# Kernel optimization log

Measured on AMD Instinct MI355X. Metric: run time of the kernel, lower is better.

Reference implementation:

```python
import jax, jax.numpy as jnp
import numpy as np
import math

B, T, D_MODEL = 1, 2048, 256
N_Q, N_KV = 16, 1
D_HEAD = D_MODEL // N_KV          # 256 (module forces d_head = d_model // n_kv_heads)
QPG = N_Q // N_KV                 # 16
ROPE_BASE = 10000.0
WINDOW = 512
EPS = 1.1920929e-07               # torch finfo(float32).eps (nn.RMSNorm default eps=None)
NEG = -1e30


def _rope(x, base=ROPE_BASE):
    # x: (b, q, g, t, d); interleaved-pair rotary embedding, freq shared per pair
    t, d = x.shape[-2], x.shape[-1]
    freqs = base ** (-2.0 * jnp.arange(d // 2, dtype=jnp.float32) / d)      # (d/2,)
    theta = jnp.arange(t, dtype=jnp.float32)[:, None] * freqs[None, :]     # (t, d/2)
    cos, sin = jnp.cos(theta), jnp.sin(theta)
    x1, x2 = x[..., 0::2], x[..., 1::2]
    r1 = x1 * cos - x2 * sin
    r2 = x1 * sin + x2 * cos
    return jnp.stack([r1, r2], axis=-1).reshape(x.shape)


def _rmsnorm(x, w):
    return x * jax.lax.rsqrt(jnp.mean(x * x, axis=-1, keepdims=True) + EPS) * w


def setup_inputs() -> dict:
    key = jax.random.key(0)
    k0, k1, k2, k3 = jax.random.split(key, 4)
    x = jax.random.normal(k0, (B, T, D_MODEL), dtype=jnp.float32)
    wq = jax.random.normal(k1, (QPG * N_KV * D_HEAD, D_MODEL), dtype=jnp.float32) * 0.02
    wkv = jax.random.normal(k2, (2 * D_HEAD * N_KV, D_MODEL), dtype=jnp.float32) * 0.02
    wo = jax.random.normal(k3, (D_MODEL, D_HEAD * N_Q * N_KV), dtype=jnp.float32) * 0.02
    q_norm_w = jnp.ones((D_HEAD,), dtype=jnp.float32)
    k_norm_w = jnp.ones((D_HEAD,), dtype=jnp.float32)
    return {"x": x, "wq": wq, "wkv": wkv, "wo": wo,
            "q_norm_w": q_norm_w, "k_norm_w": k_norm_w}


def reference(x, wq, wkv, wo, q_norm_w, k_norm_w):
    Bx, Tx, C = x.shape
    q = x @ wq.T                                  # (b, t, qpg*n_kv*d_head)
    kv = x @ wkv.T                                # (b, t, 2*n_kv*d_head)
    k, v = kv[..., :N_KV * D_HEAD], kv[..., N_KV * D_HEAD:]
    # b t q g d -> b q g t d
    q = q.reshape(Bx, Tx, QPG, N_KV, D_HEAD).transpose(0, 2, 3, 1, 4)
    k = k.reshape(Bx, Tx, 1, N_KV, D_HEAD).transpose(0, 2, 3, 1, 4)
    v = v.reshape(Bx, Tx, 1, N_KV, D_HEAD).transpose(0, 2, 3, 1, 4)
    q = _rmsnorm(_rope(q), q_norm_w)
    k = _rmsnorm(_rope(k), k_norm_w)
    rows = jnp.arange(Tx)[:, None]
    cols = jnp.arange(Tx)[None, :]
    mask = (cols <= rows) & ((rows - cols) <= WINDOW)           # causal & sliding window
    scale = 1.0 / math.sqrt(D_HEAD)
    scores = jnp.einsum('bqgtd,bqgsd->bqgts', q, k) * scale     # (b, qpg, n_kv, t, t)
    scores = jnp.where(mask[None, None, None], scores, NEG)
    attn = jax.nn.softmax(scores, axis=-1)
    out = jnp.einsum('bqgts,bqgsd->bqgtd', attn, v)
    out = out.transpose(0, 3, 1, 2, 4).reshape(Bx, Tx, QPG * N_KV * D_HEAD)  # b t (q g d)
    return out @ wo.T
```

## Files before the change

### kernel.cpp

```cpp
#include <hip/hip_runtime.h>

#define TT   2048
#define WIN  512

typedef unsigned short u16;
typedef unsigned long long u64;
typedef __bf16 bf16x8 __attribute__((ext_vector_type(8)));
typedef float  f32x4  __attribute__((ext_vector_type(4)));

__device__ __forceinline__ float bf2f(u16 u){
  unsigned v = ((unsigned)u) << 16;
  return __builtin_bit_cast(float, v);
}
__device__ __forceinline__ u16 f2bf(float f){
  unsigned x = __builtin_bit_cast(unsigned, f);
  unsigned r = x + 0x7fffu + ((x >> 16) & 1u);
  return (u16)(r >> 16);
}
__device__ __forceinline__ f32x4 mfma16(bf16x8 a, bf16x8 b, f32x4 c){
  return __builtin_amdgcn_mfma_f32_16x16x32_bf16(a, b, c, 0, 0, 0);
}
__device__ __forceinline__ bf16x8 ld512(const u16* buf, int row, int byte){
  return *(const bf16x8*)((const char*)buf + row*512 + (byte ^ ((row&7)<<4)));
}
__device__ __forceinline__ bf16x8 ld128(const u16* buf, int row, int byte){
  return *(const bf16x8*)((const char*)buf + row*128 + (byte ^ ((row&7)<<4)));
}
#define GL16(gp, lp) __builtin_amdgcn_global_load_lds( \
    (const __attribute__((address_space(1))) unsigned int*)(gp), \
    (__attribute__((address_space(3))) unsigned int*)(lp), 16, 0, 0)

__global__ __launch_bounds__(64) void k_detect(const u16* __restrict__ x, int* __restrict__ flag){
  int lane = threadIdx.x;
  float mx = 0.f;
  for (int i = lane; i < 2048; i += 64){
    float v = fabsf(bf2f(x[i]));
    mx = (v < 64.0f) ? fmaxf(mx, v) : 1e30f;
  }
  #pragma unroll
  for (int d = 32; d; d >>= 1) mx = fmaxf(mx, __shfl_xor(mx, d));
  if (lane == 0) *flag = (mx < 64.0f) ? 1 : 0;
}

__global__ __launch_bounds__(256) void k_prep(const void* __restrict__ x_r, const void* __restrict__ wq_r,
                                              const void* __restrict__ wkv_r, const void* __restrict__ wo_r,
                                              const void* __restrict__ qw_r, const void* __restrict__ kw_r,
                                              u16* __restrict__ xb, u16* __restrict__ wqb,
                                              u16* __restrict__ wkvb, u16* __restrict__ wob,
                                              float* __restrict__ tab, float* __restrict__ qwf,
                                              float* __restrict__ kwf, const int* __restrict__ flag){
  int b = blockIdx.x, t = threadIdx.x;
  if (b < 1024){
    int idx = b*256 + t;
    int tt = idx >> 7, i = idx & 127;
    float fr = exp2f((float)i * (-13.287712379549449f / 128.0f));
    float th = (float)tt * fr;
    tab[idx*2 + 0] = cosf(th);
    tab[idx*2 + 1] = sinf(th);
    return;
  }
  if (b == 3712){
    int f = *flag;
    qwf[t] = f ? bf2f(((const u16*)qw_r)[t]) : ((const float*)qw_r)[t];
    kwf[t] = f ? bf2f(((const u16*)kw_r)[t]) : ((const float*)kw_r)[t];
    return;
  }
  if (*flag) return;
  int cb = b - 1024;
  const float* s; u16* d; int i;
  if (cb < 512)       { s=(const float*)x_r;   d=xb;   i = cb*256 + t; }
  else if (cb < 1536) { s=(const float*)wq_r;  d=wqb;  i = (cb-512)*256 + t; }
  else if (cb < 1664) { s=(const float*)wkv_r; d=wkvb; i = (cb-1536)*256 + t; }
  else                { s=(const float*)wo_r;  d=wob;  i = (cb-1664)*256 + t; }
  float4 v = *(const float4*)(s + (size_t)i*4);
  u64 pk = (u64)f2bf(v.x) | ((u64)f2bf(v.y)<<16) | ((u64)f2bf(v.z)<<32) | ((u64)f2bf(v.w)<<48);
  *(u64*)(d + (size_t)i*4) = pk;
}

__global__ __launch_bounds__(256) void k_qkv(const u16* __restrict__ xb, const u16* __restrict__ wqb,
                                             const u16* __restrict__ wkvb,
                                             const void* __restrict__ x_r, const void* __restrict__ wq_r,
                                             const void* __restrict__ wkv_r, const int* __restrict__ flag,
                                             u16* __restrict__ q_raw, u16* __restrict__ kv_raw){
  __shared__ __align__(16) u16 Ax[64*256];
  __shared__ __align__(16) u16 Bw[64*256];
  int fl = *flag;
  const u16* x   = fl ? (const u16*)x_r   : xb;
  const u16* wq  = fl ? (const u16*)wq_r  : wqb;
  const u16* wkv = fl ? (const u16*)wkv_r : wkvb;
  int m0 = blockIdx.x * 64, n0 = blockIdx.y * 64;
  int tid = threadIdx.x;
  const u16* wsrc = (n0 < 4096) ? (wq + (size_t)n0*256) : (wkv + (size_t)(n0-4096)*256);
  int sr = tid >> 5, sk = tid & 31;
  #pragma unroll
  for (int u=0;u<8;++u){
    int r = sr + u*8;
    uint4 a = *(const uint4*)((const char*)(x    + (size_t)(m0+r)*256) + sk*16);
    uint4 b = *(const uint4*)((const char*)(wsrc + (size_t)r*256)      + sk*16);
    *(uint4*)((char*)&Ax[0] + r*512 + ((sk*16) ^ ((r&7)<<4))) = a;
    *(uint4*)((char*)&Bw[0] + r*512 + ((sk*16) ^ ((r&7)<<4))) = b;
  }
  __syncthreads();
  int w = tid>>6, lane = tid&63, ml = lane&15, g = lane>>4;
  int mh = w & 1, nh = w >> 1;
  f32x4 acc[2][2];
  #pragma unroll
  for (int mr=0;mr<2;++mr)
    #pragma unroll
    for (int j=0;j<2;++j) acc[mr][j] = f32x4{0.f,0.f,0.f,0.f};
  #pragma unroll
  for (int kk=0; kk<8; ++kk){
    bf16x8 af[2], bf[2];
    #pragma unroll
    for (int mr=0;mr<2;++mr) af[mr] = ld512(Ax, mh*32 + mr*16 + ml, kk*64 + g*16);
    #pragma unroll
    for (int j=0;j<2;++j)    bf[j]  = ld512(Bw, nh*32 + j*16 + ml,  kk*64 + g*16);
    #pragma unroll
    for (int mr=0;mr<2;++mr)
      #pragma unroll
      for (int j=0;j<2;++j) acc[mr][j] = mfma16(af[mr], bf[j], acc[mr][j]);
  }
  #pragma unroll
  for (int mr=0;mr<2;++mr)
    #pragma unroll
    for (int j=0;j<2;++j)
      #pragma unroll
      for (int r=0;r<4;++r){
        int row = m0 + mh*32 + mr*16 + 4*g + r;
        int n   = n0 + nh*32 + j*16 + ml;
        float v = acc[mr][j][r];
        if (n < 4096) q_raw[(size_t)row*4096 + n] = f2bf(v);
        else          kv_raw[(size_t)row*512 + (n - 4096)] = f2bf(v);
      }
}

__device__ __forceinline__ void rope_norm_row(const u16* __restrict__ src, const float* __restrict__ tab,
                                              const float* __restrict__ wn, u16* __restrict__ dst,
                                              int lane, float post){
  union { u64 q; u16 u[4]; } iv;
  iv.q = *(const u64*)(src + lane*4);
  float v0 = bf2f(iv.u[0]), v1 = bf2f(iv.u[1]), v2 = bf2f(iv.u[2]), v3 = bf2f(iv.u[3]);
  float4 tc = *(const float4*)(tab + lane*4);
  float r0 = v0*tc.x - v1*tc.y;
  float r1 = v0*tc.y + v1*tc.x;
  float r2 = v2*tc.z - v3*tc.w;
  float r3 = v2*tc.w + v3*tc.z;
  float ss = r0*r0 + r1*r1 + r2*r2 + r3*r3;
  #pragma unroll
  for (int d=32; d; d>>=1) ss += __shfl_xor(ss, d);
  float sc = rsqrtf(ss * (1.0f/256.0f) + 1.1920929e-07f) * post;
  u64 pk =  (u64)f2bf(r0*sc*wn[lane*4+0])
         | ((u64)f2bf(r1*sc*wn[lane*4+1]) << 16)
         | ((u64)f2bf(r2*sc*wn[lane*4+2]) << 32)
         | ((u64)f2bf(r3*sc*wn[lane*4+3]) << 48);
  *(u64*)(dst + lane*4) = pk;
}

__global__ __launch_bounds__(256) void k_ropenorm(const u16* __restrict__ q_raw, const u16* __restrict__ kv_raw,
                                                  const float* __restrict__ tab, const float* __restrict__ qw,
                                                  const float* __restrict__ kw, u16* __restrict__ qn,
                                                  u16* __restrict__ kn){
  int row  = blockIdx.x * 4 + (threadIdx.x >> 6);
  int lane = threadIdx.x & 63;
  if (row < 16*2048){
    int h = row >> 11, t = row & 2047;
    rope_norm_row(q_raw + (size_t)t*4096 + h*256, tab + (size_t)t*256, qw,
                  qn + ((size_t)h*2048 + t)*256, lane, 0.0625f);
  } else {
    int t = row - 16*2048;
    rope_norm_row(kv_raw + (size_t)t*512, tab + (size_t)t*256, kw, kn + (size_t)t*256, lane, 1.0f);
  }
}

__global__ __launch_bounds__(256) void k_vtrans(const u16* __restrict__ kv_raw, u16* __restrict__ vt){
  __shared__ u16 Ts[64][72];
  int t0 = blockIdx.x*64, d0 = blockIdx.y*64;
  int tid = threadIdx.x;
  int rr = tid >> 3, c8 = (tid & 7) * 8;
  #pragma unroll
  for (int u=0;u<2;++u){
    int r = rr + u*32;
    uint4 v = *(const uint4*)(kv_raw + (size_t)(t0+r)*512 + 256 + d0 + c8);
    #pragma unroll
    for (int i=0;i<8;++i) Ts[r][c8+i] = ((const u16*)&v)[i];
  }
  __syncthreads();
  #pragma unroll
  for (int u=0;u<2;++u){
    int d = rr + u*32;
    u16 tmp[8];
    #pragma unroll
    for (int i=0;i<8;++i) tmp[i] = Ts[c8+i][d];
    *(uint4*)(vt + (size_t)(d0+d)*2048 + t0 + c8) = *(uint4*)tmp;
  }
}

__global__ __launch_bounds__(512, 2) void k_attn(const u16* __restrict__ qn, const u16* __restrict__ kn,
                                                 const u16* __restrict__ vt, u16* __restrict__ aout){
  __shared__ __align__(16) u16 S[73728];
  int h = blockIdx.x >> 4, qt = blockIdx.x & 15;
  int Q0 = qt * 128;
  int tid = threadIdx.x, w = tid >> 6, lane = tid & 63, ml = lane & 15, g = lane >> 4;
  u16* Pw = S + 65536 + w*1024;
  int s_lo = Q0 - WIN; if (s_lo < 0) s_lo = 0;
  int ntile = (Q0 + 128 - s_lo) >> 6;

  bf16x8 qf[8];
  {
    const u16* qp = qn + ((size_t)h*2048 + Q0 + w*16 + ml)*256 + 8*g;
    #pragma unroll
    for (int kk=0; kk<8; ++kk) qf[kk] = *(const bf16x8*)(qp + kk*32);
  }

  int krl = lane >> 5, kslot = lane & 31;
  int vrl = lane >> 3, vslot = lane & 7;

  {
    int s0 = s_lo;
    #pragma unroll
    for (int i=0;i<4;++i){
      int r = w*8 + i*2 + krl;
      GL16(kn + (size_t)(s0 + r)*256 + ((kslot ^ (r&7))*8), S + (w*8 + i*2)*256);
    }
    #pragma unroll
    for (int i=0;i<4;++i){
      int d = w*32 + i*8 + vrl;
      GL16(vt + (size_t)d*2048 + s0 + ((vslot ^ (d&7))*8), S + 32768 + (w*32 + i*8)*64);
    }
  }

  float mx = -1e30f, ls = 0.f;
  f32x4 o[16];
  #pragma unroll
  for (int f=0; f<16; ++f) o[f] = f32x4{0.f,0.f,0.f,0.f};
  int tq = Q0 + w*16 + ml;
  int wmin = Q0 + w*16, wmax = wmin + 15;
  int cur = 0;

  for (int kt=0; kt<ntile; ++kt){
    int s0 = s_lo + kt*64;
    if (kt+1 < ntile){
      int s1 = s0 + 64, nx = cur ^ 1;
      #pragma unroll
      for (int i=0;i<4;++i){
        int r = w*8 + i*2 + krl;
        GL16(kn + (size_t)(s1 + r)*256 + ((kslot ^ (r&7))*8), S + nx*16384 + (w*8 + i*2)*256);
      }
      #pragma unroll
      for (int i=0;i<4;++i){
        int d = w*32 + i*8 + vrl;
        GL16(vt + (size_t)d*2048 + s1 + ((vslot ^ (d&7))*8), S + 32768 + nx*16384 + (w*32 + i*8)*64);
      }
      asm volatile("s_waitcnt vmcnt(8)" ::: "memory");
    } else {
      asm volatile("s_waitcnt vmcnt(0)" ::: "memory");
    }
    __builtin_amdgcn_s_barrier();
    __builtin_amdgcn_sched_barrier(0);

    bool act = (s0 <= wmax) && (s0 + 63 + WIN >= wmin);
    if (act){
      const u16* kb = S + cur*16384;
      const u16* vb = S + 32768 + cur*16384;
      f32x4 s2[4];
      #pragma unroll
      for (int j=0;j<4;++j) s2[j] = f32x4{0.f,0.f,0.f,0.f};
      __builtin_amdgcn_s_setprio(1);
      #pragma unroll
      for (int kk=0; kk<8; ++kk)
        #pragma unroll
        for (int j=0;j<4;++j)
          s2[j] = mfma16(ld512(kb, j*16 + ml, kk*64 + g*16), qf[kk], s2[j]);
      __builtin_amdgcn_s_setprio(0);
      float best = -1e30f;
      #pragma unroll
      for (int j=0;j<4;++j)
        #pragma unroll
        for (int r=0;r<4;++r){
          int key = s0 + j*16 + 4*g + r;
          float v = s2[j][r];
          bool ok = (key <= tq) && (tq - key <= WIN);
          v = ok ? v : -1e30f;
          s2[j][r] = v;
          best = fmaxf(best, v);
        }
      best = fmaxf(best, __shfl_xor(best, 16));
      best = fmaxf(best, __shfl_xor(best, 32));
      if (__ballot(best > mx + 8.f)){
        float mn = fmaxf(mx, best);
        float corr = __expf(mx - mn);
        mx = mn; ls *= corr;
        #pragma unroll
        for (int f=0; f<16; ++f) o[f] *= corr;
      }
      float rs = 0.f;
      #pragma unroll
      for (int j=0;j<4;++j){
        u64 pk = 0;
        #pragma unroll
        for (int r=0;r<4;++r){
          float v = s2[j][r];
          float p = (v <= -1e29f) ? 0.f : __expf(v - mx);
          rs += p;
          pk |= (u64)f2bf(p) << (16*r);
        }
        *(u64*)((char*)Pw + ml*128 + ((j*32 + 8*g) ^ ((ml&7)<<4))) = pk;
      }
      rs += __shfl_xor(rs, 16);
      rs += __shfl_xor(rs, 32);
      ls += rs;
      __builtin_amdgcn_s_setprio(1);
      #pragma unroll
      for (int kk2=0; kk2<2; ++kk2){
        bf16x8 pb = ld128(Pw, ml, kk2*64 + g*16);
        #pragma unroll
        for (int f=0; f<16; ++f){
          bf16x8 vf = ld128(vb, f*16 + ml, kk2*64 + g*16);
          o[f] = mfma16(vf, pb, o[f]);
        }
      }
      __builtin_amdgcn_s_setprio(0);
    }
    __builtin_amdgcn_s_barrier();
    __builtin_amdgcn_sched_barrier(0);
    cur ^= 1;
  }
  float inv = 1.0f / ls;
  u16* dst = aout + ((size_t)h*2048 + tq)*256;
  #pragma unroll
  for (int f=0; f<16; ++f){
    f32x4 v = o[f];
    u64 pk = (u64)f2bf(v[0]*inv) | ((u64)f2bf(v[1]*inv)<<16)
           | ((u64)f2bf(v[2]*inv)<<32) | ((u64)f2bf(v[3]*inv)<<48);
    *(u64*)(dst + f*16 + 4*g) = pk;
  }
}

__global__ __launch_bounds__(256) void k_oproj(const u16* __restrict__ aout, const u16* __restrict__ wob,
                                               const void* __restrict__ wo_r, const int* __restrict__ flag,
                                               float* __restrict__ pout){
  __shared__ __align__(16) u16 As[64*256];
  __shared__ __align__(16) u16 Bs[64*256];
  const u16* wo = *flag ? (const u16*)wo_r : wob;
  int t0 = blockIdx.x * 64, c0 = blockIdx.y * 64, ksp = blockIdx.z;
  int tid = threadIdx.x, w = tid>>6, lane = tid&63, ml = lane&15, g = lane>>4;
  int mh = w & 1, nh = w >> 1;
  int sr = tid >> 5, sk = tid & 31;
  f32x4 acc[2][2];
  #pragma unroll
  for (int mr=0;mr<2;++mr)
    #pragma unroll
    for (int j=0;j<2;++j) acc[mr][j] = f32x4{0.f,0.f,0.f,0.f};
  for (int kc = ksp*4; kc < ksp*4 + 4; ++kc){
    __syncthreads();
    #pragma unroll
    for (int u=0;u<8;++u){
      int r = sr + u*8;
      uint4 a = *(const uint4*)((const char*)(aout + ((size_t)kc*2048 + t0 + r)*256) + sk*16);
      uint4 b = *(const uint4*)((const char*)(wo + (size_t)(c0+r)*4096 + kc*256) + sk*16);
      *(uint4*)((char*)&As[0] + r*512 + ((sk*16) ^ ((r&7)<<4))) = a;
      *(uint4*)((char*)&Bs[0] + r*512 + ((sk*16) ^ ((r&7)<<4))) = b;
    }
    __syncthreads();
    #pragma unroll
    for (int kk=0; kk<8; ++kk){
      bf16x8 af[2], bf[2];
      #pragma unroll
      for (int mr=0;mr<2;++mr) af[mr] = ld512(As, mh*32 + mr*16 + ml, kk*64 + g*16);
      #pragma unroll
      for (int j=0;j<2;++j)    bf[j]  = ld512(Bs, nh*32 + j*16 + ml,  kk*64 + g*16);
      #pragma unroll
      for (int mr=0;mr<2;++mr)
        #pragma unroll
        for (int j=0;j<2;++j) acc[mr][j] = mfma16(af[mr], bf[j], acc[mr][j]);
    }
  }
  #pragma unroll
  for (int mr=0;mr<2;++mr)
    #pragma unroll
    for (int j=0;j<2;++j)
      #pragma unroll
      for (int r=0;r<4;++r){
        int t = t0 + mh*32 + mr*16 + 4*g + r;
        int c = c0 + nh*32 + j*16 + ml;
        pout[((size_t)ksp*2048 + t)*256 + c] = acc[mr][j][r];
      }
}

__global__ __launch_bounds__(256) void k_red(const float* __restrict__ pout, void* __restrict__ out,
                                             const int* __restrict__ flag){
  int i = blockIdx.x * 256 + threadIdx.x;
  float v = pout[i] + pout[i + 2048*256] + pout[i + 2*2048*256] + pout[i + 3*2048*256];
  if (*flag) ((u16*)out)[i] = f2bf(v);
  else       ((float*)out)[i] = v;
}

extern "C" void kernel_launch(void* const* d_in, const int* in_sizes, int n_in,
                              void* d_out, int out_size, void* d_ws, size_t ws_size,
                              hipStream_t stream) {
  (void)in_sizes; (void)n_in; (void)out_size; (void)ws_size;
  const void* x_r   = d_in[0];
  const void* wq_r  = d_in[1];
  const void* wkv_r = d_in[2];
  const void* wo_r  = d_in[3];
  const void* qw_r  = d_in[4];
  const void* kw_r  = d_in[5];
  char* ws = (char*)d_ws;
  const size_t MB = 1048576;
  u16*   xb     = (u16*)  (ws);
  u16*   wqb    = (u16*)  (ws + 1*MB);
  u16*   wkvb   = (u16*)  (ws + 3*MB);
  u16*   wob    = (u16*)  (ws + 3*MB + MB/2);
  float* tab    = (float*)(ws + 5*MB + MB/2);
  u16*   q_raw  = (u16*)  (ws + 7*MB + MB/2);
  u16*   aout   = q_raw;
  u16*   kv_raw = (u16*)  (ws + 23*MB + MB/2);
  u16*   qn     = (u16*)  (ws + 25*MB + MB/2);
  float* pout   = (float*)qn;
  u16*   kn     = (u16*)  (ws + 41*MB + MB/2);
  u16*   vt     = (u16*)  (ws + 42*MB + MB/2);
  int*   flag   = (int*)  (ws + 43*MB + MB/2);
  float* qwf    = (float*)(ws + 43*MB + MB/2 + 256);
  float* kwf    = (float*)(ws + 43*MB + MB/2 + 1280);

  k_detect<<<dim3(1),    dim3(64),  0, stream>>>((const u16*)x_r, flag);
  k_prep  <<<dim3(3713), dim3(256), 0, stream>>>(x_r, wq_r, wkv_r, wo_r, qw_r, kw_r,
                                                 xb, wqb, wkvb, wob, tab, qwf, kwf, flag);
  k_qkv     <<<dim3(32, 72),   dim3(256), 0, stream>>>(xb, wqb, wkvb, x_r, wq_r, wkv_r, flag,
                                                       q_raw, kv_raw);
  k_ropenorm<<<dim3(8704),     dim3(256), 0, stream>>>(q_raw, kv_raw, tab, qwf, kwf, qn, kn);
  k_vtrans  <<<dim3(32, 4),    dim3(256), 0, stream>>>(kv_raw, vt);
  k_attn    <<<dim3(256),      dim3(512), 0, stream>>>(qn, kn, vt, aout);
  k_oproj   <<<dim3(32, 4, 4), dim3(256), 0, stream>>>(aout, wob, wo_r, flag, pout);
  k_red     <<<dim3(2048),     dim3(256), 0, stream>>>(pout, d_out, flag);
}
```

Before: 100.1 us.

## Fuse Q rope+norm into attention, write V transposed from QKV GEMM

Q-side rotary embedding and RMS norm now run inside the attention kernel's prologue, straight from the raw projection output. This removes a full pass that wrote and reread the 16-head normalized Q tensor. The QKV GEMM epilogue writes V directly in transposed layout, so the separate transpose kernel goes away, and the K-only norm becomes a small dedicated kernel. The cost is more work and register pressure in the attention prologue, plus strided scattered 2-byte stores for V in the GEMM epilogue.

```diff
diff --git a/kernel.cpp b/kernel.cpp
--- a/kernel.cpp
+++ b/kernel.cpp
@@ -81,7 +81,8 @@
                                              const u16* __restrict__ wkvb,
                                              const void* __restrict__ x_r, const void* __restrict__ wq_r,
                                              const void* __restrict__ wkv_r, const int* __restrict__ flag,
-                                             u16* __restrict__ q_raw, u16* __restrict__ kv_raw){
+                                             u16* __restrict__ q_raw, u16* __restrict__ kv_raw,
+                                             u16* __restrict__ vt){
   __shared__ __align__(16) u16 Ax[64*256];
   __shared__ __align__(16) u16 Bw[64*256];
   int fl = *flag;
@@ -129,18 +130,22 @@
         int row = m0 + mh*32 + mr*16 + 4*g + r;
         int n   = n0 + nh*32 + j*16 + ml;
         float v = acc[mr][j][r];
-        if (n < 4096) q_raw[(size_t)row*4096 + n] = f2bf(v);
-        else          kv_raw[(size_t)row*512 + (n - 4096)] = f2bf(v);
-      }
-}
-
-__device__ __forceinline__ void rope_norm_row(const u16* __restrict__ src, const float* __restrict__ tab,
-                                              const float* __restrict__ wn, u16* __restrict__ dst,
-                                              int lane, float post){
+        u16 bv = f2bf(v);
+        if (n < 4096)      q_raw[(size_t)row*4096 + n] = bv;
+        else if (n < 4352) kv_raw[(size_t)row*256 + (n - 4096)] = bv;
+        else               vt[(size_t)(n - 4352)*2048 + row] = bv;
+      }
+}
+
+__global__ __launch_bounds__(256) void k_knorm(const u16* __restrict__ kv_raw, const float* __restrict__ tab,
+                                               const float* __restrict__ kwf, u16* __restrict__ kn){
+  int row  = blockIdx.x * 4 + (threadIdx.x >> 6);
+  int lane = threadIdx.x & 63;
+  const u16* src = kv_raw + (size_t)row*256;
   union { u64 q; u16 u[4]; } iv;
   iv.q = *(const u64*)(src + lane*4);
   float v0 = bf2f(iv.u[0]), v1 = bf2f(iv.u[1]), v2 = bf2f(iv.u[2]), v3 = bf2f(iv.u[3]);
-  float4 tc = *(const float4*)(tab + lane*4);
+  float4 tc = *(const float4*)(tab + (size_t)row*256 + lane*4);
   float r0 = v0*tc.x - v1*tc.y;
   float r1 = v0*tc.y + v1*tc.x;
   float r2 = v2*tc.z - v3*tc.w;
@@ -148,55 +153,17 @@
   float ss = r0*r0 + r1*r1 + r2*r2 + r3*r3;
   #pragma unroll
   for (int d=32; d; d>>=1) ss += __shfl_xor(ss, d);
-  float sc = rsqrtf(ss * (1.0f/256.0f) + 1.1920929e-07f) * post;
-  u64 pk =  (u64)f2bf(r0*sc*wn[lane*4+0])
-         | ((u64)f2bf(r1*sc*wn[lane*4+1]) << 16)
-         | ((u64)f2bf(r2*sc*wn[lane*4+2]) << 32)
-         | ((u64)f2bf(r3*sc*wn[lane*4+3]) << 48);
-  *(u64*)(dst + lane*4) = pk;
-}
-
-__global__ __launch_bounds__(256) void k_ropenorm(const u16* __restrict__ q_raw, const u16* __restrict__ kv_raw,
-                                                  const float* __restrict__ tab, const float* __restrict__ qw,
-                                                  const float* __restrict__ kw, u16* __restrict__ qn,
-                                                  u16* __restrict__ kn){
-  int row  = blockIdx.x * 4 + (threadIdx.x >> 6);
-  int lane = threadIdx.x & 63;
-  if (row < 16*2048){
-    int h = row >> 11, t = row & 2047;
-    rope_norm_row(q_raw + (size_t)t*4096 + h*256, tab + (size_t)t*256, qw,
-                  qn + ((size_t)h*2048 + t)*256, lane, 0.0625f);
-  } else {
-    int t = row - 16*2048;
-    rope_norm_row(kv_raw + (size_t)t*512, tab + (size_t)t*256, kw, kn + (size_t)t*256, lane, 1.0f);
-  }
-}
-
-__global__ __launch_bounds__(256) void k_vtrans(const u16* __restrict__ kv_raw, u16* __restrict__ vt){
-  __shared__ u16 Ts[64][72];
-  int t0 = blockIdx.x*64, d0 = blockIdx.y*64;
-  int tid = threadIdx.x;
-  int rr = tid >> 3, c8 = (tid & 7) * 8;
-  #pragma unroll
-  for (int u=0;u<2;++u){
-    int r = rr + u*32;
-    uint4 v = *(const uint4*)(kv_raw + (size_t)(t0+r)*512 + 256 + d0 + c8);
-    #pragma unroll
-    for (int i=0;i<8;++i) Ts[r][c8+i] = ((const u16*)&v)[i];
-  }
-  __syncthreads();
-  #pragma unroll
-  for (int u=0;u<2;++u){
-    int d = rr + u*32;
-    u16 tmp[8];
-    #pragma unroll
-    for (int i=0;i<8;++i) tmp[i] = Ts[c8+i][d];
-    *(uint4*)(vt + (size_t)(d0+d)*2048 + t0 + c8) = *(uint4*)tmp;
-  }
-}
-
-__global__ __launch_bounds__(512, 2) void k_attn(const u16* __restrict__ qn, const u16* __restrict__ kn,
-                                                 const u16* __restrict__ vt, u16* __restrict__ aout){
+  float sc = rsqrtf(ss * (1.0f/256.0f) + 1.1920929e-07f);
+  u64 pk =  (u64)f2bf(r0*sc*kwf[lane*4+0])
+         | ((u64)f2bf(r1*sc*kwf[lane*4+1]) << 16)
+         | ((u64)f2bf(r2*sc*kwf[lane*4+2]) << 32)
+         | ((u64)f2bf(r3*sc*kwf[lane*4+3]) << 48);
+  *(u64*)(kn + (size_t)row*256 + lane*4) = pk;
+}
+
+__global__ __launch_bounds__(512, 2) void k_attn(const u16* __restrict__ q_raw, const u16* __restrict__ kn,
+                                                 const u16* __restrict__ vt, const float* __restrict__ tab,
+                                                 const float* __restrict__ qwf, u16* __restrict__ aout){
   __shared__ __align__(16) u16 S[73728];
   int h = blockIdx.x >> 4, qt = blockIdx.x & 15;
   int Q0 = qt * 128;
@@ -204,13 +171,8 @@
   u16* Pw = S + 65536 + w*1024;
   int s_lo = Q0 - WIN; if (s_lo < 0) s_lo = 0;
   int ntile = (Q0 + 128 - s_lo) >> 6;
-
-  bf16x8 qf[8];
-  {
-    const u16* qp = qn + ((size_t)h*2048 + Q0 + w*16 + ml)*256 + 8*g;
-    #pragma unroll
-    for (int kk=0; kk<8; ++kk) qf[kk] = *(const bf16x8*)(qp + kk*32);
-  }
+  int tq = Q0 + w*16 + ml;
+  int wmin = Q0 + w*16, wmax = wmin + 15;
 
   int krl = lane >> 5, kslot = lane & 31;
   int vrl = lane >> 3, vslot = lane & 7;
@@ -229,12 +191,51 @@
     }
   }
 
+  bf16x8 qf[8];
+  {
+    const u16* qp = q_raw + (size_t)tq*4096 + h*256;
+    const float* tp = tab + (size_t)tq*256;
+    float rf[8][8];
+    float ss = 0.f;
+    #pragma unroll
+    for (int kk=0; kk<8; ++kk){
+      int c0 = kk*32 + 8*g;
+      union { u64 q[2]; u16 u[8]; } iv;
+      iv.q[0] = *(const u64*)(qp + c0);
+      iv.q[1] = *(const u64*)(qp + c0 + 4);
+      float4 t0 = *(const float4*)(tp + c0);
+      float4 t1 = *(const float4*)(tp + c0 + 4);
+      float tc[8] = {t0.x,t0.y,t0.z,t0.w,t1.x,t1.y,t1.z,t1.w};
+      #pragma unroll
+      for (int p=0; p<4; ++p){
+        float a = bf2f(iv.u[2*p]), b = bf2f(iv.u[2*p+1]);
+        float cc = tc[2*p], sn = tc[2*p+1];
+        float r0 = a*cc - b*sn;
+        float r1 = a*sn + b*cc;
+        rf[kk][2*p] = r0; rf[kk][2*p+1] = r1;
+        ss += r0*r0 + r1*r1;
+      }
+    }
+    ss += __shfl_xor(ss, 16);
+    ss += __shfl_xor(ss, 32);
+    float sc = rsqrtf(ss * (1.0f/256.0f) + 1.1920929e-07f) * 0.0625f;
+    #pragma unroll
+    for (int kk=0; kk<8; ++kk){
+      int c0 = kk*32 + 8*g;
+      float4 w0 = *(const float4*)(qwf + c0);
+      float4 w1 = *(const float4*)(qwf + c0 + 4);
+      float wv[8] = {w0.x,w0.y,w0.z,w0.w,w1.x,w1.y,w1.z,w1.w};
+      union { u16 u[8]; bf16x8 v; } pk;
+      #pragma unroll
+      for (int e=0; e<8; ++e) pk.u[e] = f2bf(rf[kk][e] * sc * wv[e]);
+      qf[kk] = pk.v;
+    }
+  }
+
   float mx = -1e30f, ls = 0.f;
   f32x4 o[16];
   #pragma unroll
   for (int f=0; f<16; ++f) o[f] = f32x4{0.f,0.f,0.f,0.f};
-  int tq = Q0 + w*16 + ml;
-  int wmin = Q0 + w*16, wmax = wmin + 15;
   int cur = 0;
 
   for (int kt=0; kt<ntile; ++kt){
@@ -413,10 +414,9 @@
   u16*   wob    = (u16*)  (ws + 3*MB + MB/2);
   float* tab    = (float*)(ws + 5*MB + MB/2);
   u16*   q_raw  = (u16*)  (ws + 7*MB + MB/2);
-  u16*   aout   = q_raw;
+  float* pout   = (float*)q_raw;
   u16*   kv_raw = (u16*)  (ws + 23*MB + MB/2);
-  u16*   qn     = (u16*)  (ws + 25*MB + MB/2);
-  float* pout   = (float*)qn;
+  u16*   aout   = (u16*)  (ws + 25*MB + MB/2);
   u16*   kn     = (u16*)  (ws + 41*MB + MB/2);
   u16*   vt     = (u16*)  (ws + 42*MB + MB/2);
   int*   flag   = (int*)  (ws + 43*MB + MB/2);
@@ -426,11 +426,10 @@
   k_detect<<<dim3(1),    dim3(64),  0, stream>>>((const u16*)x_r, flag);
   k_prep  <<<dim3(3713), dim3(256), 0, stream>>>(x_r, wq_r, wkv_r, wo_r, qw_r, kw_r,
                                                  xb, wqb, wkvb, wob, tab, qwf, kwf, flag);
-  k_qkv     <<<dim3(32, 72),   dim3(256), 0, stream>>>(xb, wqb, wkvb, x_r, wq_r, wkv_r, flag,
-                                                       q_raw, kv_raw);
-  k_ropenorm<<<dim3(8704),     dim3(256), 0, stream>>>(q_raw, kv_raw, tab, qwf, kwf, qn, kn);
-  k_vtrans  <<<dim3(32, 4),    dim3(256), 0, stream>>>(kv_raw, vt);
-  k_attn    <<<dim3(256),      dim3(512), 0, stream>>>(qn, kn, vt, aout);
-  k_oproj   <<<dim3(32, 4, 4), dim3(256), 0, stream>>>(aout, wob, wo_r, flag, pout);
-  k_red     <<<dim3(2048),     dim3(256), 0, stream>>>(pout, d_out, flag);
-}
+  k_qkv   <<<dim3(32, 72),   dim3(256), 0, stream>>>(xb, wqb, wkvb, x_r, wq_r, wkv_r, flag,
+                                                     q_raw, kv_raw, vt);
+  k_knorm <<<dim3(512),      dim3(256), 0, stream>>>(kv_raw, tab, kwf, kn);
+  k_attn  <<<dim3(256),      dim3(512), 0, stream>>>(q_raw, kn, vt, tab, qwf, aout);
+  k_oproj <<<dim3(32, 4, 4), dim3(256), 0, stream>>>(aout, wob, wo_r, flag, pout);
+  k_red   <<<dim3(2048),     dim3(256), 0, stream>>>(pout, d_out, flag);
+}
```

Measured after the change: 96.10 us. 1.04x faster.
